# Performance work log

Hardware: AMD Instinct MI355X
Metric: run time of the kernel (lower is better)

The kernel has to match this reference:

```python
import jax, jax.numpy as jnp
import numpy as np

N_NODES = 50000
N_EDGES = 800000
N_GRAPHS = 64


def setup_inputs() -> dict:
    key = jax.random.key(0)
    ks = jax.random.split(key, 12)

    def w(k, shape):
        fan_in = shape[0]
        return jax.random.normal(k, shape, dtype=jnp.float32) / np.sqrt(fan_in)

    x = jax.random.normal(ks[0], (N_NODES, 6), dtype=jnp.float32)
    edge_index = jax.random.randint(ks[1], (2, N_EDGES), 0, N_NODES, dtype=jnp.int64)
    batch = jnp.sort(jax.random.randint(ks[2], (N_NODES,), 0, N_GRAPHS, dtype=jnp.int64))
    return {
        "x": x,
        "edge_index": edge_index,
        "batch": batch,
        "W_in": w(ks[3], (6, 64)),
        "b_in": jnp.zeros((64,), jnp.float32),
        "W1": w(ks[4], (64, 128)),
        "b1": jnp.zeros((128,), jnp.float32),
        "W2": w(ks[5], (128, 128)),
        "b2": jnp.zeros((128,), jnp.float32),
        "Wp": w(ks[6], (256, 256)),
        "bp": jnp.zeros((256,), jnp.float32),
    }


def reference(x, edge_index, batch, W_in, b_in, W1, b1, W2, b2, Wp, bp):
    n = x.shape[0]
    self_loop = jnp.arange(n, dtype=edge_index.dtype)
    src = jnp.concatenate([edge_index[0], self_loop])  # [E+N]
    dst = jnp.concatenate([edge_index[1], self_loop])
    # GCN symmetric normalization with self-loops (PyG GCNConv default)
    deg = jax.ops.segment_sum(jnp.ones_like(dst, x.dtype), dst, num_segments=n)
    dinv = jax.lax.rsqrt(deg)  # deg >= 1 because of self-loops
    norm = (dinv[src] * dinv[dst])[:, None]  # [E+N, 1]

    def gcn(h, W, b):
        hw = h @ W                       # linear first, like GCNConv
        msg = hw[src] * norm             # gather + normalize per edge
        return jax.ops.segment_sum(msg, dst, num_segments=n) + b

    h = x @ W_in + b_in                  # input_projection
    h = jax.nn.relu(gcn(h, W1, b1))      # relu(gnn1(...))
    h = jax.nn.relu(gcn(h, W2, b2))      # relu(gnn2(...))

    # global mean / max pooling over batch segments
    counts = jax.ops.segment_sum(jnp.ones((n,), h.dtype), batch, num_segments=N_GRAPHS)
    h_mean = jax.ops.segment_sum(h, batch, num_segments=N_GRAPHS) / jnp.maximum(counts, 1.0)[:, None]
    h_max = jax.ops.segment_max(h, batch, num_segments=N_GRAPHS)
    h_max = jnp.where(counts[:, None] > 0, h_max, 0.0)
    h_graph = jnp.concatenate([h_mean, h_max], axis=1)  # [G, 256]

    # projection MLP: Linear + ReLU (Dropout is identity in eval)
    return jax.nn.relu(h_graph @ Wp + bp)
```

## Files before the change

kernel.cpp:

```cpp
#include <hip/hip_runtime.h>
#include <hip/hip_fp16.h>

#define N_NODES 50000
#define N_EDGES 800000
#define N_GRAPHS 64
#define N_PAD 50048

#define CB 256
#define EPB (N_EDGES / CB)
#define NBUCKET ((N_NODES + 255) / 256)

typedef _Float16 f16x8 __attribute__((ext_vector_type(8)));
typedef float f32x4 __attribute__((ext_vector_type(4)));
typedef float f32x2 __attribute__((ext_vector_type(2)));


__global__ void k_prep(const float* __restrict__ W_in, const float* __restrict__ b_in,
                       const float* __restrict__ W1, const float* __restrict__ W2,
                       _Float16* __restrict__ Wt2, float* __restrict__ Wcz,
                       float* psum, float* pmax, int* totals, int* gcursor,
                       const int* __restrict__ batch, float* __restrict__ pcnt) {
    int idx = blockIdx.x * blockDim.x + threadIdx.x;
    if (idx < 128 * 128) {
        int n = idx >> 7, k = idx & 127;
        Wt2[idx] = (_Float16)(W2[k * 128 + n] * 0.03125f);
    } else if (idx < 128 * 128 + 1024) {
        int j = idx - 128 * 128;
        int ch = j >> 3, k = j & 7;
        float acc = 0.f;
        if (k < 6) {
            for (int q = 0; q < 64; q++) acc += W_in[k * 64 + q] * W1[q * 128 + ch];
        } else if (k == 6) {
            for (int q = 0; q < 64; q++) acc += b_in[q] * W1[q * 128 + ch];
        }
        Wcz[k * 128 + ch] = acc;
    }
    if (idx < N_GRAPHS * 128) { psum[idx] = 0.f; pmax[idx] = 0.f; }
    if (idx < 256) { totals[idx] = 0; gcursor[idx] = 0; }
    if (blockIdx.x == 0) {
        __shared__ int shp[N_GRAPHS + 1];
        int tt = threadIdx.x;
        if (tt <= N_GRAPHS) {
            int lo = 0, hi = N_NODES;
            while (lo < hi) {
                int mid = (lo + hi) >> 1;
                if (batch[mid] < tt) lo = mid + 1; else hi = mid;
            }
            shp[tt] = lo;
        }
        __syncthreads();
        if (tt < N_GRAPHS) pcnt[tt] = (float)(shp[tt + 1] - shp[tt]);
    }
}


__global__ __launch_bounds__(256) void k_coarse_hist(const int* __restrict__ dst,
                                                     int* __restrict__ totals) {
    __shared__ int hist[NBUCKET];
    int t = threadIdx.x, b = blockIdx.x;
    for (int i = t; i < NBUCKET; i += 256) hist[i] = 0;
    __syncthreads();
    int e0 = b * EPB;
    for (int e = e0 + t; e < e0 + EPB; e += 256)
        atomicAdd(&hist[dst[e] >> 8], 1);
    __syncthreads();
    for (int i = t; i < NBUCKET; i += 256)
        if (hist[i] > 0) atomicAdd(&totals[i], hist[i]);
}

__global__ __launch_bounds__(256) void k_scan_scatter(
        const int* __restrict__ src, const int* __restrict__ dst,
        const int* __restrict__ totals, int* __restrict__ bucket_base,
        int* __restrict__ gcursor, unsigned int* __restrict__ esort) {
    __shared__ int cur[256];
    __shared__ int sc[256];
    int t = threadIdx.x, b = blockIdx.x;
    cur[t] = 0;
    __syncthreads();
    int e0 = b * EPB;
    for (int e = e0 + t; e < e0 + EPB; e += 256)
        atomicAdd(&cur[dst[e] >> 8], 1);
    __syncthreads();
    int lcnt = cur[t];
    int v = (t < NBUCKET) ? totals[t] : 0;
    sc[t] = v;
    __syncthreads();
    for (int off = 1; off < 256; off <<= 1) {
        int u = (t >= off) ? sc[t - off] : 0;
        __syncthreads();
        sc[t] += u;
        __syncthreads();
    }
    int base = sc[t] - v;
    int off = (t < NBUCKET && lcnt > 0) ? atomicAdd(&gcursor[t], lcnt) : 0;
    cur[t] = base + off;
    if (b == 0) {
        if (t < NBUCKET) bucket_base[t] = base;
        if (t == 0) bucket_base[NBUCKET] = N_EDGES;
    }
    __syncthreads();
    for (int e = e0 + t; e < e0 + EPB; e += 256) {
        int d = dst[e];
        int slot = atomicAdd(&cur[d >> 8], 1);
        esort[slot] = ((unsigned)(d & 255) << 16) | (unsigned)src[e];
    }
}

__global__ __launch_bounds__(256) void k_fine_fill_p(
        const unsigned int* __restrict__ esort, const int* __restrict__ bucket_base,
        int* __restrict__ col, int* __restrict__ row_ptr, float* __restrict__ dinv,
        const float* __restrict__ x, float* __restrict__ p) {
    __shared__ int hist[256];
    __shared__ int sc[256];
    __shared__ int cur[256];
    int t = threadIdx.x, b = blockIdx.x;
    hist[t] = 0;
    __syncthreads();
    int base = bucket_base[b], end = bucket_base[b + 1];
    for (int e = base + t; e < end; e += 256)
        atomicAdd(&hist[(esort[e] >> 16) & 255], 1);
    __syncthreads();
    int v = hist[t];
    sc[t] = v;
    __syncthreads();
    for (int off = 1; off < 256; off <<= 1) {
        int u = (t >= off) ? sc[t - off] : 0;
        __syncthreads();
        sc[t] += u;
        __syncthreads();
    }
    int start = base + sc[t] - v;
    cur[t] = start;
    int node = b * 256 + t;
    float di = rsqrtf((float)(v + 1));
    if (node < N_NODES) {
        row_ptr[node] = start;
        dinv[node] = di;
        float pr[8];
#pragma unroll
        for (int k = 0; k < 6; k++) pr[k] = x[node * 6 + k] * di;
        pr[6] = di;
        pr[7] = 0.f;
        *(f32x4*)&p[(size_t)node * 8] = *(f32x4*)&pr[0];
        *(f32x4*)&p[(size_t)node * 8 + 4] = *(f32x4*)&pr[4];
    }
    if (b == 0 && t == 0) row_ptr[N_NODES] = N_EDGES;
    __syncthreads();
    for (int e = base + t; e < end; e += 256) {
        unsigned pk = esort[e];
        int slot = atomicAdd(&cur[(pk >> 16) & 255], 1);
        col[slot] = (int)(pk & 0xffffu);
    }
}

__global__ __launch_bounds__(256, 8) void k_agg_proj(
        const float* __restrict__ p, const int* __restrict__ row_ptr,
        const int* __restrict__ col, const float* __restrict__ Wcz,
        const float* __restrict__ b1, const float* __restrict__ dinv,
        unsigned char* __restrict__ g1, int n) {
    __shared__ float tl[32][8];
    __shared__ float Wl[8 * 128];
    __shared__ float bl[128];
    int t = threadIdx.x;
    for (int i = t; i < 1024; i += 256) Wl[i] = Wcz[i];
    if (t < 128) bl[t] = b1[t];

    int rg = t >> 3, ck = t & 7;
    int row = blockIdx.x * 32 + rg;
    float acc = 0.f;
    if (row < n) {
        acc = p[(size_t)row * 8 + ck];
        int e = row_ptr[row], e1 = row_ptr[row + 1];
        for (; e + 3 < e1; e += 4) {
            int c0 = col[e], c1 = col[e + 1], c2 = col[e + 2], c3 = col[e + 3];
            float v0 = p[(size_t)c0 * 8 + ck];
            float v1 = p[(size_t)c1 * 8 + ck];
            float v2 = p[(size_t)c2 * 8 + ck];
            float v3 = p[(size_t)c3 * 8 + ck];
            acc += (v0 + v1) + (v2 + v3);
        }
        for (; e < e1; e++) acc += p[(size_t)col[e] * 8 + ck];
    }
    tl[rg][ck] = acc;
    __syncthreads();

    int rg2 = t >> 3, oc = t & 7;
    int row2 = blockIdx.x * 32 + rg2;
    if (row2 < n) {
        float tr[7];
#pragma unroll
        for (int k = 0; k < 7; k++) tr[k] = tl[rg2][k];
        float di = dinv[row2];
        float hv[16];
#pragma unroll
        for (int c = 0; c < 16; c++) {
            int ch = oc * 16 + c;
            float z = 0.f;
#pragma unroll
            for (int k = 0; k < 7; k++) z += tr[k] * Wl[k * 128 + ch];
            z = di * z + bl[ch];
            hv[c] = fmaxf(z, 0.f) * di * 32.f;
        }
        unsigned w[4];
#pragma unroll
        for (int q = 0; q < 4; q++) {
            int word = 0;
            word = __builtin_amdgcn_cvt_pk_fp8_f32(hv[q * 4 + 0], hv[q * 4 + 1], word, false);
            word = __builtin_amdgcn_cvt_pk_fp8_f32(hv[q * 4 + 2], hv[q * 4 + 3], word, true);
            w[q] = (unsigned)word;
        }
        *(uint4*)&g1[(size_t)row2 * 128 + oc * 16] = make_uint4(w[0], w[1], w[2], w[3]);
    }
}

__global__ __launch_bounds__(256, 8) void k_gnn2f8(
        const unsigned char* __restrict__ g, const int* __restrict__ row_ptr,
        const int* __restrict__ col, const _Float16* __restrict__ Wt2,
        const float* __restrict__ b2, const float* __restrict__ dinv,
        const int* __restrict__ batch, float* __restrict__ psum,
        float* __restrict__ pmax, int n) {
    constexpr int ROWS = 16, KP = 136;
    __shared__ __align__(16) char smem[ROWS * 128 * 4];
    _Float16* Sl = (_Float16*)smem;
    float* Hs = (float*)smem;
    int t = threadIdx.x;

    {
        int rl = t >> 4, ck = t & 15;
        int row = blockIdx.x * ROWS + rl;
        f32x2 aA[4] = {};
        f32x2 aB[4] = {};
        const uint2* gb = (const uint2*)g;
        auto addv = [](f32x2* acc, uint2 w) {
            acc[0] += __builtin_amdgcn_cvt_pk_f32_fp8((int)w.x, false);
            acc[1] += __builtin_amdgcn_cvt_pk_f32_fp8((int)w.x, true);
            acc[2] += __builtin_amdgcn_cvt_pk_f32_fp8((int)w.y, false);
            acc[3] += __builtin_amdgcn_cvt_pk_f32_fp8((int)w.y, true);
        };
        if (row < n) {
            addv(aA, gb[(size_t)row * 16 + ck]);
            int e = row_ptr[row], e1 = row_ptr[row + 1];
            for (; e + 3 < e1; e += 4) {
                int c0 = col[e], c1 = col[e + 1], c2 = col[e + 2], c3 = col[e + 3];
                uint2 v0 = gb[(size_t)c0 * 16 + ck];
                uint2 v1 = gb[(size_t)c1 * 16 + ck];
                uint2 v2 = gb[(size_t)c2 * 16 + ck];
                uint2 v3 = gb[(size_t)c3 * 16 + ck];
                addv(aA, v0);
                addv(aB, v1);
                addv(aA, v2);
                addv(aB, v3);
            }
            if (e + 1 < e1) {
                uint2 v0 = gb[(size_t)col[e] * 16 + ck];
                uint2 v1 = gb[(size_t)col[e + 1] * 16 + ck];
                addv(aA, v0);
                addv(aB, v1);
                e += 2;
            }
            if (e < e1) addv(aA, gb[(size_t)col[e] * 16 + ck]);
        }
        f16x8 o;
#pragma unroll
        for (int j = 0; j < 4; j++) {
            o[2 * j] = (_Float16)(aA[j].x + aB[j].x);
            o[2 * j + 1] = (_Float16)(aA[j].y + aB[j].y);
        }
        *(f16x8*)&Sl[rl * KP + ck * 8] = o;
    }
    __syncthreads();

    int wave = t >> 6;
    int lane = t & 63;
    int m = lane & 15;
    int quad = lane >> 4;
    int col_base = wave * 32;

    f32x4 acc[2] = {};
#pragma unroll
    for (int k0 = 0; k0 < 128; k0 += 32) {
        f16x8 a = *(const f16x8*)&Sl[m * KP + k0 + quad * 8];
#pragma unroll
        for (int ct = 0; ct < 2; ct++) {
            f16x8 bw = *(const f16x8*)(Wt2 + (size_t)(col_base + ct * 16 + m) * 128
                                       + k0 + quad * 8);
            acc[ct] = __builtin_amdgcn_mfma_f32_16x16x32_f16(a, bw, acc[ct], 0, 0, 0);
        }
    }

    __syncthreads();
#pragma unroll
    for (int r = 0; r < 4; r++) {
        int rl = quad * 4 + r;
        int row = blockIdx.x * ROWS + rl;
        float di = (row < n) ? dinv[row] : 0.f;
#pragma unroll
        for (int ct = 0; ct < 2; ct++) {
            int colb = col_base + ct * 16 + m;
            float v = fmaxf(di * acc[ct][r] + b2[colb], 0.f);
            Hs[rl * 128 + colb] = (row < n) ? v : 0.f;
        }
    }
    __syncthreads();
    if (t < 128) {
        int colb = t;
        int row0b = blockIdx.x * ROWS;
        float s = 0.f, mx = 0.f;
        int gcur = batch[row0b < n ? row0b : (n - 1)];
        for (int rr = 0; rr < ROWS; rr++) {
            int row = row0b + rr;
            if (row >= n) break;
            int gi = batch[row];
            if (gi != gcur) {
                atomicAdd(&psum[gcur * 128 + colb], s);
                atomicMax((int*)&pmax[gcur * 128 + colb], __float_as_int(mx));
                s = 0.f; mx = 0.f; gcur = gi;
            }
            float v = Hs[rr * 128 + colb];
            s += v;
            mx = fmaxf(mx, v);
        }
        atomicAdd(&psum[gcur * 128 + colb], s);
        atomicMax((int*)&pmax[gcur * 128 + colb], __float_as_int(mx));
    }
}


__global__ void k_final(const float* __restrict__ psum, const float* __restrict__ pmax,
                        const float* __restrict__ pcnt, const float* __restrict__ Wp,
                        const float* __restrict__ bp, float* __restrict__ out) {
    int t = blockIdx.x * blockDim.x + threadIdx.x;
    if (t >= N_GRAPHS * 256) return;
    int g = t >> 8, j = t & 255;
    float inv = 1.0f / fmaxf(pcnt[g], 1.0f);
    float acc = bp[j];
#pragma unroll 4
    for (int k = 0; k < 128; k++) acc += (psum[g * 128 + k] * inv) * Wp[k * 256 + j];
#pragma unroll 4
    for (int k = 0; k < 128; k++) acc += pmax[g * 128 + k] * Wp[(128 + k) * 256 + j];
    out[t] = fmaxf(acc, 0.f);
}

extern "C" void kernel_launch(void* const* d_in, const int* in_sizes, int n_in,
                              void* d_out, int out_size, void* d_ws, size_t ws_size,
                              hipStream_t stream) {
    const int N = N_NODES, E = N_EDGES;
    const float* x    = (const float*)d_in[0];
    const int*   ei   = (const int*)d_in[1];
    const int*   src  = ei;
    const int*   dst  = ei + E;
    const int*   batch= (const int*)d_in[2];
    const float* W_in = (const float*)d_in[3];
    const float* b_in = (const float*)d_in[4];
    const float* W1   = (const float*)d_in[5];
    const float* b1   = (const float*)d_in[6];
    const float* W2   = (const float*)d_in[7];
    const float* b2   = (const float*)d_in[8];
    const float* Wp   = (const float*)d_in[9];
    const float* bp   = (const float*)d_in[10];
    float* out = (float*)d_out;

    char* p8 = (char*)d_ws;
    int* totals      = (int*)p8;   p8 += 256 * 4;
    int* bucket_base = (int*)p8;   p8 += 256 * 4;
    int* gcursor     = (int*)p8;   p8 += 256 * 4;
    int* row_ptr     = (int*)p8;   p8 += (N_PAD + 64) * 4;
    int* col         = (int*)p8;   p8 += (size_t)N_EDGES * 4;
    unsigned* esort  = (unsigned*)p8; p8 += (size_t)N_EDGES * 4;
    float* dinv      = (float*)p8; p8 += N_PAD * 4;
    float* Wcz       = (float*)p8; p8 += 1024 * 4;
    _Float16* Wt2    = (_Float16*)p8; p8 += 128 * 128 * 2;
    float* pfeat     = (float*)p8; p8 += (size_t)N_PAD * 8 * 4;
    unsigned char* g1f8 = (unsigned char*)p8; p8 += (size_t)N_PAD * 128;
    float* psum      = (float*)p8; p8 += N_GRAPHS * 128 * 4;
    float* pmax      = (float*)p8; p8 += N_GRAPHS * 128 * 4;
    float* pcnt      = (float*)p8;

    const int TB = 256;
    dim3 blk(TB);

    k_prep<<<(128 * 128 + 1024 + TB - 1) / TB, blk, 0, stream>>>(
        W_in, b_in, W1, W2, Wt2, Wcz, psum, pmax, totals, gcursor, batch, pcnt);

    k_coarse_hist<<<CB, blk, 0, stream>>>(dst, totals);
    k_scan_scatter<<<CB, blk, 0, stream>>>(src, dst, totals, bucket_base, gcursor, esort);
    k_fine_fill_p<<<NBUCKET, blk, 0, stream>>>(esort, bucket_base, col, row_ptr, dinv,
                                               x, pfeat);

    k_agg_proj<<<(N + 31) / 32, blk, 0, stream>>>(pfeat, row_ptr, col, Wcz, b1, dinv,
                                                  g1f8, N);

    k_gnn2f8<<<(N + 15) / 16, blk, 0, stream>>>(
        g1f8, row_ptr, col, Wt2, b2, dinv, batch, psum, pmax, N);

    k_final<<<(N_GRAPHS * 256 + TB - 1) / TB, blk, 0, stream>>>(psum, pmax, pcnt, Wp, bp, out);
}
```

Baseline: 186.0 us.

## Drop coarse histogram pass by scattering edges into fixed-capacity buckets

```diff
diff --git a/kernel.cpp b/kernel.cpp
--- a/kernel.cpp
+++ b/kernel.cpp
@@ -9,6 +9,7 @@
 #define CB 256
 #define EPB (N_EDGES / CB)
 #define NBUCKET ((N_NODES + 255) / 256)
+#define BCAP 5120
 
 typedef _Float16 f16x8 __attribute__((ext_vector_type(8)));
 typedef float f32x4 __attribute__((ext_vector_type(4)));
@@ -18,7 +19,7 @@
 __global__ void k_prep(const float* __restrict__ W_in, const float* __restrict__ b_in,
                        const float* __restrict__ W1, const float* __restrict__ W2,
                        _Float16* __restrict__ Wt2, float* __restrict__ Wcz,
-                       float* psum, float* pmax, int* totals, int* gcursor,
+                       float* psum, float* pmax, int* gcursor,
                        const int* __restrict__ batch, float* __restrict__ pcnt) {
     int idx = blockIdx.x * blockDim.x + threadIdx.x;
     if (idx < 128 * 128) {
@@ -36,7 +37,7 @@
         Wcz[k * 128 + ch] = acc;
     }
     if (idx < N_GRAPHS * 128) { psum[idx] = 0.f; pmax[idx] = 0.f; }
-    if (idx < 256) { totals[idx] = 0; gcursor[idx] = 0; }
+    if (idx < 256) gcursor[idx] = 0;
     if (blockIdx.x == 0) {
         __shared__ int shp[N_GRAPHS + 1];
         int tt = threadIdx.x;
@@ -53,27 +54,10 @@
     }
 }
 
-
-__global__ __launch_bounds__(256) void k_coarse_hist(const int* __restrict__ dst,
-                                                     int* __restrict__ totals) {
-    __shared__ int hist[NBUCKET];
-    int t = threadIdx.x, b = blockIdx.x;
-    for (int i = t; i < NBUCKET; i += 256) hist[i] = 0;
-    __syncthreads();
-    int e0 = b * EPB;
-    for (int e = e0 + t; e < e0 + EPB; e += 256)
-        atomicAdd(&hist[dst[e] >> 8], 1);
-    __syncthreads();
-    for (int i = t; i < NBUCKET; i += 256)
-        if (hist[i] > 0) atomicAdd(&totals[i], hist[i]);
-}
-
 __global__ __launch_bounds__(256) void k_scan_scatter(
         const int* __restrict__ src, const int* __restrict__ dst,
-        const int* __restrict__ totals, int* __restrict__ bucket_base,
         int* __restrict__ gcursor, unsigned int* __restrict__ esort) {
     __shared__ int cur[256];
-    __shared__ int sc[256];
     int t = threadIdx.x, b = blockIdx.x;
     cur[t] = 0;
     __syncthreads();
@@ -82,22 +66,8 @@
         atomicAdd(&cur[dst[e] >> 8], 1);
     __syncthreads();
     int lcnt = cur[t];
-    int v = (t < NBUCKET) ? totals[t] : 0;
-    sc[t] = v;
-    __syncthreads();
-    for (int off = 1; off < 256; off <<= 1) {
-        int u = (t >= off) ? sc[t - off] : 0;
-        __syncthreads();
-        sc[t] += u;
-        __syncthreads();
-    }
-    int base = sc[t] - v;
     int off = (t < NBUCKET && lcnt > 0) ? atomicAdd(&gcursor[t], lcnt) : 0;
-    cur[t] = base + off;
-    if (b == 0) {
-        if (t < NBUCKET) bucket_base[t] = base;
-        if (t == 0) bucket_base[NBUCKET] = N_EDGES;
-    }
+    cur[t] = t * BCAP + off;
     __syncthreads();
     for (int e = e0 + t; e < e0 + EPB; e += 256) {
         int d = dst[e];
@@ -107,18 +77,31 @@
 }
 
 __global__ __launch_bounds__(256) void k_fine_fill_p(
-        const unsigned int* __restrict__ esort, const int* __restrict__ bucket_base,
+        const unsigned int* __restrict__ esort, const int* __restrict__ gcursor,
         int* __restrict__ col, int* __restrict__ row_ptr, float* __restrict__ dinv,
         const float* __restrict__ x, float* __restrict__ p) {
     __shared__ int hist[256];
     __shared__ int sc[256];
     __shared__ int cur[256];
+    __shared__ int bb[2];
     int t = threadIdx.x, b = blockIdx.x;
+    int tv = (t < NBUCKET) ? gcursor[t] : 0;
+    sc[t] = tv;
+    __syncthreads();
+    for (int off = 1; off < 256; off <<= 1) {
+        int u = (t >= off) ? sc[t - off] : 0;
+        __syncthreads();
+        sc[t] += u;
+        __syncthreads();
+    }
+    if (t == b) { bb[0] = sc[t] - tv; bb[1] = tv; }
     hist[t] = 0;
     __syncthreads();
-    int base = bucket_base[b], end = bucket_base[b + 1];
-    for (int e = base + t; e < end; e += 256)
-        atomicAdd(&hist[(esort[e] >> 16) & 255], 1);
+    int base = bb[0];
+    size_t sbase = (size_t)b * BCAP;
+    int total = bb[1];
+    for (int e = t; e < total; e += 256)
+        atomicAdd(&hist[(esort[sbase + e] >> 16) & 255], 1);
     __syncthreads();
     int v = hist[t];
     sc[t] = v;
@@ -146,8 +129,8 @@
     }
     if (b == 0 && t == 0) row_ptr[N_NODES] = N_EDGES;
     __syncthreads();
-    for (int e = base + t; e < end; e += 256) {
-        unsigned pk = esort[e];
+    for (int e = t; e < total; e += 256) {
+        unsigned pk = esort[sbase + e];
         int slot = atomicAdd(&cur[(pk >> 16) & 255], 1);
         col[slot] = (int)(pk & 0xffffu);
     }
@@ -361,12 +344,10 @@
     float* out = (float*)d_out;
 
     char* p8 = (char*)d_ws;
-    int* totals      = (int*)p8;   p8 += 256 * 4;
-    int* bucket_base = (int*)p8;   p8 += 256 * 4;
     int* gcursor     = (int*)p8;   p8 += 256 * 4;
     int* row_ptr     = (int*)p8;   p8 += (N_PAD + 64) * 4;
     int* col         = (int*)p8;   p8 += (size_t)N_EDGES * 4;
-    unsigned* esort  = (unsigned*)p8; p8 += (size_t)N_EDGES * 4;
+    unsigned* esort  = (unsigned*)p8; p8 += (size_t)NBUCKET * BCAP * 4;
     float* dinv      = (float*)p8; p8 += N_PAD * 4;
     float* Wcz       = (float*)p8; p8 += 1024 * 4;
     _Float16* Wt2    = (_Float16*)p8; p8 += 128 * 128 * 2;
@@ -380,11 +361,10 @@
     dim3 blk(TB);
 
     k_prep<<<(128 * 128 + 1024 + TB - 1) / TB, blk, 0, stream>>>(
-        W_in, b_in, W1, W2, Wt2, Wcz, psum, pmax, totals, gcursor, batch, pcnt);
-
-    k_coarse_hist<<<CB, blk, 0, stream>>>(dst, totals);
-    k_scan_scatter<<<CB, blk, 0, stream>>>(src, dst, totals, bucket_base, gcursor, esort);
-    k_fine_fill_p<<<NBUCKET, blk, 0, stream>>>(esort, bucket_base, col, row_ptr, dinv,
+        W_in, b_in, W1, W2, Wt2, Wcz, psum, pmax, gcursor, batch, pcnt);
+
+    k_scan_scatter<<<CB, blk, 0, stream>>>(src, dst, gcursor, esort);
+    k_fine_fill_p<<<NBUCKET, blk, 0, stream>>>(esort, gcursor, col, row_ptr, dinv,
                                                x, pfeat);
 
     k_agg_proj<<<(N + 31) / 32, blk, 0, stream>>>(pfeat, row_ptr, col, Wcz, b1, dinv,
```

New measurement: 177.7 us. -4.5%, faster.
